# Optimization experiments

Measured on AMD Instinct MI355X. Metric: run time of the kernel, lower is better.

## Reference

```python
import jax, jax.numpy as jnp
import numpy as np

N_QUBITS = 4
DEPTH = 1
KERNEL = 2  # 2x2 windows, stride 2


def _apply_rz_batched(state, theta, wire):
    # diagonal gate: diag(e^{-i t/2}, e^{+i t/2}) per sample; theta: (N,)
    ph = jnp.exp(0.5j * theta)                      # (N,) complex64
    diag = jnp.stack([jnp.conj(ph), ph], axis=-1)   # (N, 2)
    shape = [theta.shape[0]] + [1] * N_QUBITS
    shape[wire + 1] = 2
    return state * diag.reshape(shape)


def _apply_ry_batched(state, theta, wire):
    # RY(t) = [[cos t/2, -sin t/2], [sin t/2, cos t/2]] per sample
    c = jnp.cos(0.5 * theta)
    s = jnp.sin(0.5 * theta)
    U = jnp.stack([jnp.stack([c, -s], -1), jnp.stack([s, c], -1)], -2)  # (N,2,2)
    U = U.astype(state.dtype)
    st = jnp.moveaxis(state, wire + 1, 1)           # (N, 2, ...)
    st = jnp.einsum('nij,nj...->ni...', U, st)
    return jnp.moveaxis(st, 1, wire + 1)


def _apply_ry_scalar(state, theta, wire):
    c = jnp.cos(0.5 * theta)
    s = jnp.sin(0.5 * theta)
    U = jnp.stack([jnp.stack([c, -s]), jnp.stack([s, c])]).astype(state.dtype)  # (2,2)
    st = jnp.moveaxis(state, wire + 1, 1)
    st = jnp.einsum('ij,nj...->ni...', U, st)
    return jnp.moveaxis(st, 1, wire + 1)


def _apply_crz(state, theta, control, target):
    # CRZ: RZ(theta) on target iff control bit is 1 (diagonal gate)
    ph = jnp.exp(0.5j * theta)
    one = jnp.ones((), state.dtype)
    tab = jnp.stack([jnp.stack([one, one]), jnp.stack([jnp.conj(ph), ph])])  # (bc, bt)
    a, b = control + 1, target + 1
    if a > b:
        tab = tab.T
        a, b = b, a
    shape = [1] * (N_QUBITS + 1)
    shape[a] = 2
    shape[b] = 2
    return state * tab.reshape(shape)


def _simulate(angles, weights):
    # angles: (N, 4) patch values; weights: (DEPTH, 2*N_QUBITS)
    N = angles.shape[0]
    # Hadamard on every qubit from |0000> -> all 16 amplitudes = 1/4
    state = jnp.full((N,) + (2,) * N_QUBITS, 0.25, dtype=jnp.complex64)
    # encoding: var_per_qubit = 2, gates [RZ, RY]; only qubits 0,1 get angles
    state = _apply_rz_batched(state, angles[:, 0], 0)
    state = _apply_ry_batched(state, angles[:, 1], 0)
    state = _apply_rz_batched(state, angles[:, 2], 1)
    state = _apply_ry_batched(state, angles[:, 3], 1)
    for d in range(DEPTH):
        for i in range(N_QUBITS):
            state = _apply_crz(state, weights[d, i], i, (i + 1) % N_QUBITS)
        for k in range(N_QUBITS):
            state = _apply_ry_scalar(state, weights[d, N_QUBITS + k], k)
    probs = state.real ** 2 + state.imag ** 2      # (N, 2,2,2,2)
    all_axes = tuple(range(1, N_QUBITS + 1))
    outs = []
    for q in range(N_QUBITS):
        red = tuple(a for a in all_axes if a != q + 1)
        p = probs.sum(axis=red)                    # (N, 2)
        outs.append(p[:, 0] - p[:, 1])             # <Z_q>
    return jnp.stack(outs, axis=-1)                # (N, 4)


def setup_inputs() -> dict:
    key = jax.random.key(0)
    k1, k2 = jax.random.split(key)
    x = jax.random.normal(k1, (512, 1, 64, 64), dtype=jnp.float32)
    weights = jax.random.normal(k2, (DEPTH, 2 * N_QUBITS), dtype=jnp.float32)
    return {"x": x, "weights": weights}


def reference(x, weights):
    B, C, H, W = x.shape  # C == 1
    ph, pw = H // 2, W // 2
    # row-major 2x2 stride-2 patches, flattened as [r0c0, r0c1, r1c0, r1c1]
    patches = x[:, 0].reshape(B, ph, 2, pw, 2).transpose(0, 1, 3, 2, 4)
    patches = patches.reshape(B * ph * pw, 4)
    ev = _simulate(patches, weights)               # (B*P, 4)
    return ev.reshape(B, ph * pw * 4)
```

## Files before the change

kernel.cpp:

```cpp
#include <hip/hip_runtime.h>
#include <math.h>


__global__ __launch_bounds__(256) void quanv_kernel(
    const float* __restrict__ x, const float* __restrict__ w,
    float* __restrict__ out, int total)
{
    int tid = blockIdx.x * blockDim.x + threadIdx.x;
    if (tid >= total) return;

    int b  = tid >> 10;
    int pl = tid & 1023;
    int r  = pl >> 5;
    int c  = pl & 31;

    const float* p0 = x + ((size_t)b << 12) + (r << 7) + (c << 1);
    float2 t0 = *reinterpret_cast<const float2*>(p0);
    float2 t1 = *reinterpret_cast<const float2*>(p0 + 64);

    float c0, s0, c1, s1, c2, s2, c3, s3;
    __sincosf(0.5f * t0.x, &s0, &c0);
    __sincosf(0.5f * t0.y, &s1, &c1);
    __sincosf(0.5f * t1.x, &s2, &c2);
    __sincosf(0.5f * t1.y, &s3, &c3);

    float v00r = (c1 - s1) * c0, v00i = -(c1 + s1) * s0;
    float v01r = (c1 + s1) * c0, v01i =  (c1 - s1) * s0;
    float v10r = (c3 - s3) * c2, v10i = -(c3 + s3) * s2;
    float v11r = (c3 + s3) * c2, v11i =  (c3 - s3) * s2;

    float wc[8], ws[8];
    #pragma unroll
    for (int k = 0; k < 8; ++k) {
        __sincosf(0.5f * w[k], &ws[k], &wc[k]);
    }

    float ar[16], ai[16];
    #pragma unroll
    for (int i = 0; i < 16; ++i) {
        float pr = ((i >> 3) & 1) ? v01r : v00r;
        float pi_ = ((i >> 3) & 1) ? v01i : v00i;
        float qr = ((i >> 2) & 1) ? v11r : v10r;
        float qi = ((i >> 2) & 1) ? v11i : v10i;
        ar[i] = 0.25f * (pr * qr - pi_ * qi);
        ai[i] = 0.25f * (pr * qi + pi_ * qr);
    }

    #pragma unroll
    for (int g = 0; g < 4; ++g) {
        const int cq = g, tq = (g + 1) & 3;
        const int mc = 1 << (3 - cq);
        const int mt = 1 << (3 - tq);
        #pragma unroll
        for (int i = 0; i < 16; ++i) {
            if (i & mc) {
                float pr = wc[g];
                float pim = (i & mt) ? ws[g] : -ws[g];
                float nr = ar[i] * pr - ai[i] * pim;
                float ni = ar[i] * pim + ai[i] * pr;
                ar[i] = nr; ai[i] = ni;
            }
        }
    }

    #pragma unroll
    for (int q = 0; q < 4; ++q) {
        const float cc = wc[4 + q], ss = ws[4 + q];
        const int m = 1 << (3 - q);
        #pragma unroll
        for (int i = 0; i < 16; ++i) {
            if (!(i & m)) {
                const int j = i | m;
                float x0r = ar[i], x0i = ai[i];
                float x1r = ar[j], x1i = ai[j];
                ar[i] = cc * x0r - ss * x1r;
                ai[i] = cc * x0i - ss * x1i;
                ar[j] = ss * x0r + cc * x1r;
                ai[j] = ss * x0i + cc * x1i;
            }
        }
    }

    float ev0 = 0.f, ev1 = 0.f, ev2 = 0.f, ev3 = 0.f;
    #pragma unroll
    for (int i = 0; i < 16; ++i) {
        float p = ar[i] * ar[i] + ai[i] * ai[i];
        ev0 += (i & 8) ? -p : p;
        ev1 += (i & 4) ? -p : p;
        ev2 += (i & 2) ? -p : p;
        ev3 += (i & 1) ? -p : p;
    }

    float4 o = make_float4(ev0, ev1, ev2, ev3);
    *reinterpret_cast<float4*>(out + ((size_t)tid << 2)) = o;
}

extern "C" void kernel_launch(void* const* d_in, const int* in_sizes, int n_in,
                              void* d_out, int out_size, void* d_ws, size_t ws_size,
                              hipStream_t stream) {
    const float* x = (const float*)d_in[0];
    const float* w = (const float*)d_in[1];
    float* out = (float*)d_out;

    int total = in_sizes[0] >> 2;
    int block = 256;
    int grid = (total + block - 1) / block;
    quanv_kernel<<<grid, block, 0, stream>>>(x, w, out, total);
}
```

Before: 68.33 us.

## Replace statevector simulation with closed-form expectation values, two patches per thread

Drops the 16-amplitude statevector simulation and computes each Pauli-Z expectation directly from closed-form trigonometric expressions in the patch angles and precomputed weight-dependent coefficients. Each thread now handles two adjacent patches using float4 loads and two float4 stores. This removes most of the per-patch arithmetic and register pressure. The derived formulas must exactly match the circuit, and any algebra mistake would silently give wrong outputs.

```diff
diff --git a/kernel.cpp b/kernel.cpp
--- a/kernel.cpp
+++ b/kernel.cpp
@@ -9,90 +9,76 @@
     int tid = blockIdx.x * blockDim.x + threadIdx.x;
     if (tid >= total) return;
 
-    int b  = tid >> 10;
-    int pl = tid & 1023;
-    int r  = pl >> 5;
-    int c  = pl & 31;
+    const float th0 = w[0], th1 = w[1], th2 = w[2], th3 = w[3];
+    const float t0 = w[4], t1 = w[5], t2 = w[6], t3 = w[7];
 
-    const float* p0 = x + ((size_t)b << 12) + (r << 7) + (c << 1);
-    float2 t0 = *reinterpret_cast<const float2*>(p0);
-    float2 t1 = *reinterpret_cast<const float2*>(p0 + 64);
+    const float c0h = __cosf(0.5f * th0), s0h = __sinf(0.5f * th0);
+    const float c0f = __cosf(th0),        s0f = __sinf(th0);
+    const float c1f = __cosf(th1),        c1h = __cosf(0.5f * th1);
+    const float c2f = __cosf(th2),        s2f = __sinf(th2);
+    const float c2h = __cosf(0.5f * th2);
+    const float c3f = __cosf(th3),        s3f = __sinf(th3);
+    const float c3h = __cosf(0.5f * th3), s3h = __sinf(0.5f * th3);
 
-    float c0, s0, c1, s1, c2, s2, c3, s3;
-    __sincosf(0.5f * t0.x, &s0, &c0);
-    __sincosf(0.5f * t0.y, &s1, &c1);
-    __sincosf(0.5f * t1.x, &s2, &c2);
-    __sincosf(0.5f * t1.y, &s3, &c3);
+    const float ct0 = __cosf(t0), st0 = __sinf(t0);
+    const float ct1 = __cosf(t1), st1 = __sinf(t1);
+    const float st2 = __sinf(t2);
+    const float st3 = __sinf(t3);
 
-    float v00r = (c1 - s1) * c0, v00i = -(c1 + s1) * s0;
-    float v01r = (c1 + s1) * c0, v01i =  (c1 - s1) * s0;
-    float v10r = (c3 - s3) * c2, v10i = -(c3 + s3) * s2;
-    float v11r = (c3 + s3) * c2, v11i =  (c3 - s3) * s2;
+    const float k1 = -0.5f * st0 * (1.f + c3f) * c0h;
+    const float k2 =  0.5f * st0 * s3f * c0h;
+    const float k3 =  0.5f * st0 * s3f * s0h;
+    const float k4 =  0.5f * st0 * (1.f + c3f) * s0h;
 
-    float wc[8], ws[8];
+    const float mb = 0.5f * st1 * c1h;
+    const float m1 = -mb * (1.f + c0f);
+    const float m2 = -mb * (c0f - 1.f);
+    const float m3 =  mb * s0f;
+    const float nb = 0.5f * st2 * c2h;
+    const float n0 = -nb * (1.f + c1f);
+    const float n1 = -nb * (c1f - 1.f);
+    const float p0 = -0.5f * st3 * (1.f + c2f) * c3h;
+    const float p1 =  0.5f * st3 * s2f * s3h;
+
+    int b  = tid >> 9;
+    int rm = tid & 511;
+    int r  = rm >> 4;
+    int cp = rm & 15;
+
+    const float* src = x + ((size_t)b << 12) + (r << 7) + (cp << 2);
+    float4 row0 = *reinterpret_cast<const float4*>(src);
+    float4 row1 = *reinterpret_cast<const float4*>(src + 64);
+
+    float4 o[2];
     #pragma unroll
-    for (int k = 0; k < 8; ++k) {
-        __sincosf(0.5f * w[k], &ws[k], &wc[k]);
+    for (int p = 0; p < 2; ++p) {
+        float a0 = p ? row0.z : row0.x;
+        float a1 = p ? row0.w : row0.y;
+        float a2 = p ? row1.z : row1.x;
+        float a3 = p ? row1.w : row1.y;
+
+        float sa0 = __sinf(a0), ca0 = __cosf(a0);
+        float sa1 = __sinf(a1), ca1 = __cosf(a1);
+        float sa2 = __sinf(a2), ca2 = __cosf(a2);
+        float sa3 = __sinf(a3), ca3 = __cosf(a3);
+
+        float Z0  = sa1 * ca0;
+        float X0r = ca1 * ca0;
+        float X0i = sa0;
+        float Z1  = sa3 * ca2;
+        float X1r = ca3 * ca2;
+        float X1i = sa2;
+
+        float ev0 = -ct0 * Z0 + k1 * X0r + k2 * X0i + Z1 * (k3 * X0r + k4 * X0i);
+        float ev1 = -ct1 * Z1 + m1 * X1r + m3 * X1i + Z0 * (m2 * X1r + m3 * X1i);
+        float ev2 = n0 + n1 * Z1;
+        float ev3 = p0 + p1 * Z0;
+        o[p] = make_float4(ev0, ev1, ev2, ev3);
     }
 
-    float ar[16], ai[16];
-    #pragma unroll
-    for (int i = 0; i < 16; ++i) {
-        float pr = ((i >> 3) & 1) ? v01r : v00r;
-        float pi_ = ((i >> 3) & 1) ? v01i : v00i;
-        float qr = ((i >> 2) & 1) ? v11r : v10r;
-        float qi = ((i >> 2) & 1) ? v11i : v10i;
-        ar[i] = 0.25f * (pr * qr - pi_ * qi);
-        ai[i] = 0.25f * (pr * qi + pi_ * qr);
-    }
-
-    #pragma unroll
-    for (int g = 0; g < 4; ++g) {
-        const int cq = g, tq = (g + 1) & 3;
-        const int mc = 1 << (3 - cq);
-        const int mt = 1 << (3 - tq);
-        #pragma unroll
-        for (int i = 0; i < 16; ++i) {
-            if (i & mc) {
-                float pr = wc[g];
-                float pim = (i & mt) ? ws[g] : -ws[g];
-                float nr = ar[i] * pr - ai[i] * pim;
-                float ni = ar[i] * pim + ai[i] * pr;
-                ar[i] = nr; ai[i] = ni;
-            }
-        }
-    }
-
-    #pragma unroll
-    for (int q = 0; q < 4; ++q) {
-        const float cc = wc[4 + q], ss = ws[4 + q];
-        const int m = 1 << (3 - q);
-        #pragma unroll
-        for (int i = 0; i < 16; ++i) {
-            if (!(i & m)) {
-                const int j = i | m;
-                float x0r = ar[i], x0i = ai[i];
-                float x1r = ar[j], x1i = ai[j];
-                ar[i] = cc * x0r - ss * x1r;
-                ai[i] = cc * x0i - ss * x1i;
-                ar[j] = ss * x0r + cc * x1r;
-                ai[j] = ss * x0i + cc * x1i;
-            }
-        }
-    }
-
-    float ev0 = 0.f, ev1 = 0.f, ev2 = 0.f, ev3 = 0.f;
-    #pragma unroll
-    for (int i = 0; i < 16; ++i) {
-        float p = ar[i] * ar[i] + ai[i] * ai[i];
-        ev0 += (i & 8) ? -p : p;
-        ev1 += (i & 4) ? -p : p;
-        ev2 += (i & 2) ? -p : p;
-        ev3 += (i & 1) ? -p : p;
-    }
-
-    float4 o = make_float4(ev0, ev1, ev2, ev3);
-    *reinterpret_cast<float4*>(out + ((size_t)tid << 2)) = o;
+    float* dst = out + ((size_t)tid << 3);
+    *reinterpret_cast<float4*>(dst)     = o[0];
+    *reinterpret_cast<float4*>(dst + 4) = o[1];
 }
 
 extern "C" void kernel_launch(void* const* d_in, const int* in_sizes, int n_in,
@@ -102,7 +88,7 @@
     const float* w = (const float*)d_in[1];
     float* out = (float*)d_out;
 
-    int total = in_sizes[0] >> 2;
+    int total = in_sizes[0] >> 3;
     int block = 256;
     int grid = (total + block - 1) / block;
     quanv_kernel<<<grid, block, 0, stream>>>(x, w, out, total);
```

New measurement: 60.28 us. 1.13x faster.
